# Kernel optimization log

Hardware: AMD Instinct MI355X
Metric: run time of the kernel (lower is better)

Reference implementation:

```python
import jax, jax.numpy as jnp
import numpy as np

T, B, I, H = 256, 128, 1024, 1024


def setup_inputs() -> dict:
    key = jax.random.key(0)
    ks = jax.random.split(key, 5)
    # weight init ranges per LSTMLayer.__init__ with wb=0 (no quantization):
    lim_hh = 1.0 / np.sqrt(H)
    lim_ih = 1.0 / np.sqrt(I)
    return {
        "x": jax.random.normal(ks[0], (T, B, I), dtype=jnp.float32),
        "h0": jax.random.normal(ks[1], (B, H), dtype=jnp.float32),
        "c0": jax.random.normal(ks[2], (B, H), dtype=jnp.float32),
        "W_ih": jax.random.uniform(ks[3], (4 * H, I), dtype=jnp.float32, minval=-lim_ih, maxval=lim_ih),
        "W_hh": jax.random.uniform(ks[4], (4 * H, H), dtype=jnp.float32, minval=-lim_hh, maxval=lim_hh),
        "b_ih": jnp.zeros((4 * H,), dtype=jnp.float32),   # uniform_(0, 0)
        "b_hh": jnp.ones((4 * H,), dtype=jnp.float32),    # uniform_(1, 1)
    }


def reference(x, h0, c0, W_ih, W_hh, b_ih, b_hh):
    # Standard LSTM cell, rolled over time with lax.scan.
    # gates layout follows torch LSTMCell: [i, f, g, o] chunks of size H.
    Wih_T = W_ih.T  # [I, 4H]
    Whh_T = W_hh.T  # [H, 4H]
    bias = b_ih + b_hh  # [4H]

    def step(carry, xt):
        h, c = carry  # [B,H] each
        gates = xt @ Wih_T + h @ Whh_T + bias  # [B, 4H]
        i, f, g, o = jnp.split(gates, 4, axis=-1)
        i = jax.nn.sigmoid(i)
        f = jax.nn.sigmoid(f)
        g = jnp.tanh(g)
        o = jax.nn.sigmoid(o)
        c_new = f * c + i * g
        h_new = o * jnp.tanh(c_new)
        return (h_new, c_new), h_new

    (hT, cT), ys = jax.lax.scan(step, (h0, c0), x)
    return ys, hT, cT  # ys: [T, B, H]
```

## Files before the change

### kernel.cpp

```cpp
#include <hip/hip_runtime.h>

#define T_ 256
#define B_ 128
#define I_ 1024
#define H_ 1024
#define G_ 4096
#define BH (B_*H_)
#define TB (T_*B_)

typedef float f32x4 __attribute__((ext_vector_type(4)));
typedef short bf16x8 __attribute__((ext_vector_type(8)));

__device__ inline unsigned short f2bf(float f) {
    union { float f; unsigned int u; } v; v.f = f;
    unsigned int u = v.u;
    unsigned int r = (u + 0x7fffu + ((u >> 16) & 1u)) >> 16;
    return (unsigned short)r;
}
__device__ inline float bf2f(unsigned short s) {
    union { unsigned int u; float f; } v; v.u = ((unsigned int)s) << 16;
    return v.f;
}
__device__ inline float sigmoidf_(float x) { return 1.0f / (1.0f + __expf(-x)); }
__device__ inline float tanhf_(float x) {
    x = fminf(15.0f, fmaxf(-15.0f, x));
    float e = __expf(2.0f * x);
    return (e - 1.0f) / (e + 1.0f);
}

__global__ void cvt_kernel(const float* __restrict__ src, unsigned short* __restrict__ dst, int n) {
    int i = (blockIdx.x * blockDim.x + threadIdx.x) * 4;
    int stride = gridDim.x * blockDim.x * 4;
    for (; i < n; i += stride) {
        float4 v = *reinterpret_cast<const float4*>(src + i);
        ushort4 o;
        o.x = f2bf(v.x); o.y = f2bf(v.y); o.z = f2bf(v.z); o.w = f2bf(v.w);
        *reinterpret_cast<ushort4*>(dst + i) = o;
    }
}

__global__ void bias_kernel(const float* __restrict__ a, const float* __restrict__ b, float* __restrict__ out) {
    int i = blockIdx.x * blockDim.x + threadIdx.x;
    if (i < G_) out[i] = a[i] + b[i];
}

__global__ __launch_bounds__(256) void pregemm(
    const unsigned short* __restrict__ xb,
    const unsigned short* __restrict__ wih,
    const float* __restrict__ bias,
    unsigned short* __restrict__ gx)
{
    int wgid = (blockIdx.x & 7) * 1024 + (blockIdx.x >> 3);
    int mg = wgid & 255;
    int ng = wgid >> 8;
    int m0 = mg * 128, n0 = ng * 128;
    int tid = threadIdx.x;
    int w = tid >> 6, l = tid & 63;
    int qm = (w >> 1) * 64, qn = (w & 1) * 64;
    int lr = l & 15, lk = (l >> 4) * 8, lq = l >> 4;

    const unsigned short* ap = xb  + (size_t)(m0 + qm + lr) * I_ + lk;
    const unsigned short* bp = wih + (size_t)(n0 + qn + lr) * I_ + lk;

    f32x4 acc[4][4] = {};
    #pragma unroll 4
    for (int kk = 0; kk < 32; ++kk) {
        bf16x8 a[4], b[4];
        #pragma unroll
        for (int mt = 0; mt < 4; ++mt)
            a[mt] = *reinterpret_cast<const bf16x8*>(ap + (size_t)mt * 16 * I_ + kk * 32);
        #pragma unroll
        for (int nt = 0; nt < 4; ++nt)
            b[nt] = *reinterpret_cast<const bf16x8*>(bp + (size_t)nt * 16 * I_ + kk * 32);
        #pragma unroll
        for (int mt = 0; mt < 4; ++mt)
            #pragma unroll
            for (int nt = 0; nt < 4; ++nt)
                acc[mt][nt] = __builtin_amdgcn_mfma_f32_16x16x32_bf16(a[mt], b[nt], acc[mt][nt], 0, 0, 0);
    }
    #pragma unroll
    for (int mt = 0; mt < 4; ++mt) {
        #pragma unroll
        for (int nt = 0; nt < 4; ++nt) {
            #pragma unroll
            for (int r = 0; r < 4; ++r) {
                int m = m0 + qm + mt * 16 + lq * 4 + r;
                int n = n0 + qn + nt * 16 + lr;
                gx[(size_t)m * G_ + n] = f2bf(acc[mt][nt][r] + bias[n]);
            }
        }
    }
}

__device__ __forceinline__ void group_barrier(unsigned* gbar, int step, int ing) {
    __syncthreads();
    if (threadIdx.x == 0) {
        unsigned target = (unsigned)(step * 8 + 7);
        unsigned old = __hip_atomic_fetch_add(gbar + (ing & 7) * 32, 1u,
                                              __ATOMIC_RELAXED, __HIP_MEMORY_SCOPE_AGENT);
        if (old == target) {
            unsigned mold = __hip_atomic_fetch_add(gbar + 256, 1u,
                                                   __ATOMIC_RELAXED, __HIP_MEMORY_SCOPE_AGENT);
            if (mold == target) {
                __hip_atomic_store(gbar + 288, (unsigned)(step + 1),
                                   __ATOMIC_RELAXED, __HIP_MEMORY_SCOPE_AGENT);
            }
        }
        while (__hip_atomic_load(gbar + 288, __ATOMIC_RELAXED, __HIP_MEMORY_SCOPE_AGENT)
               < (unsigned)(step + 1)) {
            __builtin_amdgcn_s_sleep(1);
        }
    }
    __syncthreads();
}

__global__ __launch_bounds__(512) void lstm_recur(
    const unsigned short* __restrict__ whh,
    const unsigned short* __restrict__ gx,
    const float* __restrict__ c0,
    unsigned short* __restrict__ hbuf,
    float* __restrict__ ys,
    float* __restrict__ hT, float* __restrict__ cT,
    unsigned* __restrict__ bar)
{
    __shared__ unsigned short whh_lds[8192 * 8];
    __shared__ float lds_g[4][32][16];

    const int bid = blockIdx.x;
    const int mg  = (bid & 7) >> 1;
    const int ing = (bid >> 3) * 2 + (bid & 1);
    const int m0 = mg * 32, n0 = ing * 16;
    unsigned* gbar = bar + mg * 512;

    const int tid = threadIdx.x;
    const int w = tid >> 6, l = tid & 63;
    const int mh = w >> 2, kq = w & 3;
    const int lr = l & 15, lkidx = l >> 4;

    for (int it = 0; it < 16; ++it) {
        int idx = it * 512 + tid;
        int row = idx >> 7;
        int ck  = idx & 127;
        int gg = row >> 4, cc = row & 15;
        bf16x8 v = *reinterpret_cast<const bf16x8*>(
            whh + (size_t)(gg * 1024 + n0 + cc) * H_ + ck * 8);
        *reinterpret_cast<bf16x8*>(whh_lds + ((size_t)ck * 64 + row) * 8) = v;
    }
    __syncthreads();

    const unsigned short* bwave = whh_lds + (((size_t)(kq * 32 + lkidx)) * 64 + lr) * 8;

    const int erow = tid >> 4, ecol = tid & 15;
    const size_t eoff = (size_t)(m0 + erow) * H_ + n0 + ecol;
    float c = c0[eoff];
    const unsigned short* gxp = gx + (size_t)(m0 + erow) * G_ + n0 + ecol;

    const size_t hrow = (size_t)(m0 + mh * 16 + lr) * H_ + kq * 256;

    unsigned short gx0 = gxp[0], gx1 = gxp[1024], gx2 = gxp[2048], gx3 = gxp[3072];

    for (int t = 0; t < T_; ++t) {
        const char* hpb = (const char*)hbuf
            + ((size_t)(t & 1) * BH + hrow) * 2 + lkidx * 16;
        bf16x8 hv0, hv1, hv2, hv3, hv4, hv5, hv6, hv7;
        asm volatile("global_load_dwordx4 %0, %1, off sc0 sc1"             : "=&v"(hv0) : "v"(hpb));
        asm volatile("global_load_dwordx4 %0, %1, off offset:64 sc0 sc1"   : "=&v"(hv1) : "v"(hpb));
        asm volatile("global_load_dwordx4 %0, %1, off offset:128 sc0 sc1"  : "=&v"(hv2) : "v"(hpb));
        asm volatile("global_load_dwordx4 %0, %1, off offset:192 sc0 sc1"  : "=&v"(hv3) : "v"(hpb));
        asm volatile("global_load_dwordx4 %0, %1, off offset:256 sc0 sc1"  : "=&v"(hv4) : "v"(hpb));
        asm volatile("global_load_dwordx4 %0, %1, off offset:320 sc0 sc1"  : "=&v"(hv5) : "v"(hpb));
        asm volatile("global_load_dwordx4 %0, %1, off offset:384 sc0 sc1"  : "=&v"(hv6) : "v"(hpb));
        asm volatile("global_load_dwordx4 %0, %1, off offset:448 sc0 sc1"  : "=&v"(hv7) : "v"(hpb));

        {
            float* lg = (float*)lds_g;
            lg[tid] = 0.f; lg[tid + 512] = 0.f; lg[tid + 1024] = 0.f; lg[tid + 1536] = 0.f;
        }

        asm volatile("s_waitcnt vmcnt(0)" ::: "memory");
        __builtin_amdgcn_sched_barrier(0);

        f32x4 acc[4] = {};
#define MFMA_K(KK, HV)                                                              \
        {                                                                           \
            _Pragma("unroll")                                                       \
            for (int g4 = 0; g4 < 4; ++g4) {                                        \
                bf16x8 bb = *reinterpret_cast<const bf16x8*>(                       \
                    bwave + (KK) * 2048 + g4 * 128);                                \
                acc[g4] = __builtin_amdgcn_mfma_f32_16x16x32_bf16(                  \
                    HV, bb, acc[g4], 0, 0, 0);                                      \
            }                                                                       \
        }
        MFMA_K(0, hv0) MFMA_K(1, hv1) MFMA_K(2, hv2) MFMA_K(3, hv3)
        MFMA_K(4, hv4) MFMA_K(5, hv5) MFMA_K(6, hv6) MFMA_K(7, hv7)
#undef MFMA_K
        __syncthreads();

        #pragma unroll
        for (int g4 = 0; g4 < 4; ++g4)
            #pragma unroll
            for (int r = 0; r < 4; ++r)
                atomicAdd(&lds_g[g4][mh * 16 + lkidx * 4 + r][lr], acc[g4][r]);
        __syncthreads();

        float gi = lds_g[0][erow][ecol] + bf2f(gx0);
        float gf = lds_g[1][erow][ecol] + bf2f(gx1);
        float gg = lds_g[2][erow][ecol] + bf2f(gx2);
        float go = lds_g[3][erow][ecol] + bf2f(gx3);
        float iv = sigmoidf_(gi);
        float fv = sigmoidf_(gf);
        float gv = tanhf_(gg);
        float ov = sigmoidf_(go);
        c = fv * c + iv * gv;
        float hn = ov * tanhf_(c);

        ys[(size_t)t * BH + eoff] = hn;

        unsigned short* hbn = hbuf + (size_t)((t + 1) & 1) * BH;
        float hn_o = __shfl_xor(hn, 1);
        if ((tid & 1) == 0) {
            unsigned u = (unsigned)f2bf(hn) | (((unsigned)f2bf(hn_o)) << 16);
            __hip_atomic_store((unsigned*)(hbn + eoff), u,
                               __ATOMIC_RELAXED, __HIP_MEMORY_SCOPE_AGENT);
        }
        if (t == T_ - 1) { hT[eoff] = hn; cT[eoff] = c; }

        if (t + 1 < T_) {
            const unsigned short* p = gxp + (size_t)(t + 1) * B_ * G_;
            gx0 = p[0]; gx1 = p[1024]; gx2 = p[2048]; gx3 = p[3072];
            group_barrier(gbar, t, ing);
        }
    }
}

extern "C" void kernel_launch(void* const* d_in, const int* in_sizes, int n_in,
                              void* d_out, int out_size, void* d_ws, size_t ws_size,
                              hipStream_t stream)
{
    const float* x   = (const float*)d_in[0];
    const float* h0  = (const float*)d_in[1];
    const float* c0  = (const float*)d_in[2];
    const float* Wih = (const float*)d_in[3];
    const float* Whh = (const float*)d_in[4];
    const float* bih = (const float*)d_in[5];
    const float* bhh = (const float*)d_in[6];

    char* ws = (char*)d_ws;
    unsigned short* gx   = (unsigned short*)(ws);
    unsigned short* xb   = (unsigned short*)(ws + 268435456);
    unsigned short* wihb = (unsigned short*)(ws + 335544320);
    unsigned short* whhb = (unsigned short*)(ws + 343932928);
    unsigned short* hbuf = (unsigned short*)(ws + 352321536);
    float*          bias = (float*)(ws + 352845824);
    unsigned*       bar  = (unsigned*)(ws + 352862208);

    float* out = (float*)d_out;
    float* ys = out;
    float* hT = out + (size_t)TB * H_;
    float* cT = hT + BH;

    hipMemsetAsync(bar, 0, 8192, stream);
    cvt_kernel<<<2048, 256, 0, stream>>>(x,   xb,   TB * I_);
    cvt_kernel<<<512,  256, 0, stream>>>(Wih, wihb, G_ * I_);
    cvt_kernel<<<512,  256, 0, stream>>>(Whh, whhb, G_ * H_);
    cvt_kernel<<<128,  256, 0, stream>>>(h0,  hbuf, BH);
    bias_kernel<<<16, 256, 0, stream>>>(bih, bhh, bias);

    pregemm<<<8192, 256, 0, stream>>>(xb, wihb, bias, gx);

    lstm_recur<<<256, 512, 0, stream>>>(whhb, gx, c0, hbuf, ys, hT, cT, bar);
}
```

Measured before the change: 4.834 ms.

## Stage pregemm tiles through LDS and replace tree barrier with per-wave counter polling

The input-projection GEMM now double-buffers A/B tiles into LDS using direct global-to-LDS loads, with two blocks per CU, instead of each wave streaming fragments straight from global memory. The recurrent kernel drops the hierarchical atomic group barrier. Each block increments one of 8 leaf counters per step, and each wave polls only the two counters covering the K-quarter of h it will read. This removes the serial master-counter hop and the block-wide wait before loading h. The trade-off is more polling traffic and dependence on relaxed-ordering visibility of the h stores. The ys store is also moved after the h publish.

```diff
diff --git a/kernel.cpp b/kernel.cpp
--- a/kernel.cpp
+++ b/kernel.cpp
@@ -26,6 +26,13 @@
     x = fminf(15.0f, fmaxf(-15.0f, x));
     float e = __expf(2.0f * x);
     return (e - 1.0f) / (e + 1.0f);
+}
+
+__device__ __forceinline__ void gload16(const unsigned short* g, unsigned short* l) {
+    __builtin_amdgcn_global_load_lds(
+        (const __attribute__((address_space(1))) void*)g,
+        (__attribute__((address_space(3))) void*)l,
+        16, 0, 0);
 }
 
 __global__ void cvt_kernel(const float* __restrict__ src, unsigned short* __restrict__ dst, int n) {
@@ -44,40 +51,70 @@
     if (i < G_) out[i] = a[i] + b[i];
 }
 
-__global__ __launch_bounds__(256) void pregemm(
+__global__ __launch_bounds__(256, 2) void pregemm(
     const unsigned short* __restrict__ xb,
     const unsigned short* __restrict__ wih,
     const float* __restrict__ bias,
     unsigned short* __restrict__ gx)
 {
-    int wgid = (blockIdx.x & 7) * 1024 + (blockIdx.x >> 3);
-    int mg = wgid & 255;
-    int ng = wgid >> 8;
+    __shared__ unsigned short Ab[2][128 * 64];
+    __shared__ unsigned short Bb[2][128 * 64];
+
+    int swz = (blockIdx.x & 7) * 1024 + (blockIdx.x >> 3);
+    int mg = swz & 255;
+    int ng = swz >> 8;
     int m0 = mg * 128, n0 = ng * 128;
     int tid = threadIdx.x;
     int w = tid >> 6, l = tid & 63;
     int qm = (w >> 1) * 64, qn = (w & 1) * 64;
-    int lr = l & 15, lk = (l >> 4) * 8, lq = l >> 4;
-
-    const unsigned short* ap = xb  + (size_t)(m0 + qm + lr) * I_ + lk;
-    const unsigned short* bp = wih + (size_t)(n0 + qn + lr) * I_ + lk;
+    int lr = l & 15, lkidx = (l >> 4);
+
+    int srow = ((w * 4) * 64 + l) >> 3;
+    int sk8  = l & 7;
+
+#define STAGE(BUF, KT)                                                              \
+    {                                                                               \
+        _Pragma("unroll")                                                           \
+        for (int it = 0; it < 4; ++it) {                                            \
+            int row = srow + it * 8;                                                \
+            gload16(xb  + (size_t)(m0 + row) * I_ + (KT) * 64 + sk8 * 8,            \
+                    &Ab[BUF][(w * 4 + it) * 512]);                                  \
+            gload16(wih + (size_t)(n0 + row) * I_ + (KT) * 64 + sk8 * 8,            \
+                    &Bb[BUF][(w * 4 + it) * 512]);                                  \
+        }                                                                           \
+    }
 
     f32x4 acc[4][4] = {};
-    #pragma unroll 4
-    for (int kk = 0; kk < 32; ++kk) {
-        bf16x8 a[4], b[4];
+    int buf = 0;
+    STAGE(0, 0)
+    __syncthreads();
+
+    for (int kt = 0; kt < 16; ++kt) {
+        if (kt + 1 < 16) STAGE(buf ^ 1, kt + 1)
         #pragma unroll
-        for (int mt = 0; mt < 4; ++mt)
-            a[mt] = *reinterpret_cast<const bf16x8*>(ap + (size_t)mt * 16 * I_ + kk * 32);
-        #pragma unroll
-        for (int nt = 0; nt < 4; ++nt)
-            b[nt] = *reinterpret_cast<const bf16x8*>(bp + (size_t)nt * 16 * I_ + kk * 32);
-        #pragma unroll
-        for (int mt = 0; mt < 4; ++mt)
+        for (int kk = 0; kk < 2; ++kk) {
+            bf16x8 a[4], b[4];
+            #pragma unroll
+            for (int mt = 0; mt < 4; ++mt)
+                a[mt] = *reinterpret_cast<const bf16x8*>(
+                    &Ab[buf][(qm + mt * 16 + lr) * 64 + kk * 32 + lkidx * 8]);
             #pragma unroll
             for (int nt = 0; nt < 4; ++nt)
-                acc[mt][nt] = __builtin_amdgcn_mfma_f32_16x16x32_bf16(a[mt], b[nt], acc[mt][nt], 0, 0, 0);
-    }
+                b[nt] = *reinterpret_cast<const bf16x8*>(
+                    &Bb[buf][(qn + nt * 16 + lr) * 64 + kk * 32 + lkidx * 8]);
+            #pragma unroll
+            for (int mt = 0; mt < 4; ++mt)
+                #pragma unroll
+                for (int nt = 0; nt < 4; ++nt)
+                    acc[mt][nt] = __builtin_amdgcn_mfma_f32_16x16x32_bf16(
+                        a[mt], b[nt], acc[mt][nt], 0, 0, 0);
+        }
+        __syncthreads();
+        buf ^= 1;
+    }
+#undef STAGE
+
+    int lq = l >> 4;
     #pragma unroll
     for (int mt = 0; mt < 4; ++mt) {
         #pragma unroll
@@ -90,28 +127,6 @@
             }
         }
     }
-}
-
-__device__ __forceinline__ void group_barrier(unsigned* gbar, int step, int ing) {
-    __syncthreads();
-    if (threadIdx.x == 0) {
-        unsigned target = (unsigned)(step * 8 + 7);
-        unsigned old = __hip_atomic_fetch_add(gbar + (ing & 7) * 32, 1u,
-                                              __ATOMIC_RELAXED, __HIP_MEMORY_SCOPE_AGENT);
-        if (old == target) {
-            unsigned mold = __hip_atomic_fetch_add(gbar + 256, 1u,
-                                                   __ATOMIC_RELAXED, __HIP_MEMORY_SCOPE_AGENT);
-            if (mold == target) {
-                __hip_atomic_store(gbar + 288, (unsigned)(step + 1),
-                                   __ATOMIC_RELAXED, __HIP_MEMORY_SCOPE_AGENT);
-            }
-        }
-        while (__hip_atomic_load(gbar + 288, __ATOMIC_RELAXED, __HIP_MEMORY_SCOPE_AGENT)
-               < (unsigned)(step + 1)) {
-            __builtin_amdgcn_s_sleep(1);
-        }
-    }
-    __syncthreads();
 }
 
 __global__ __launch_bounds__(512) void lstm_recur(
@@ -130,12 +145,14 @@
     const int mg  = (bid & 7) >> 1;
     const int ing = (bid >> 3) * 2 + (bid & 1);
     const int m0 = mg * 32, n0 = ing * 16;
-    unsigned* gbar = bar + mg * 512;
 
     const int tid = threadIdx.x;
     const int w = tid >> 6, l = tid & 63;
     const int mh = w >> 2, kq = w & 3;
     const int lr = l & 15, lkidx = l >> 4;
+
+    const unsigned* pollw = bar + mg * 32 + 2 * kq;
+    unsigned* leafw = bar + mg * 32 + (ing >> 3);
 
     for (int it = 0; it < 16; ++it) {
         int idx = it * 512 + tid;
@@ -160,6 +177,18 @@
     unsigned short gx0 = gxp[0], gx1 = gxp[1024], gx2 = gxp[2048], gx3 = gxp[3072];
 
     for (int t = 0; t < T_; ++t) {
+        if (t > 0) {
+            unsigned tgt = 8u * (unsigned)t;
+            while (true) {
+                unsigned long long lv;
+                asm volatile("global_load_dwordx2 %0, %1, off sc0 sc1"
+                             : "=&v"(lv) : "v"(pollw));
+                asm volatile("s_waitcnt vmcnt(0)" ::: "memory");
+                if ((unsigned)lv >= tgt && (unsigned)(lv >> 32) >= tgt) break;
+                __builtin_amdgcn_s_sleep(1);
+            }
+        }
+
         const char* hpb = (const char*)hbuf
             + ((size_t)(t & 1) * BH + hrow) * 2 + lkidx * 16;
         bf16x8 hv0, hv1, hv2, hv3, hv4, hv5, hv6, hv7;
@@ -214,8 +243,6 @@
         c = fv * c + iv * gv;
         float hn = ov * tanhf_(c);
 
-        ys[(size_t)t * BH + eoff] = hn;
-
         unsigned short* hbn = hbuf + (size_t)((t + 1) & 1) * BH;
         float hn_o = __shfl_xor(hn, 1);
         if ((tid & 1) == 0) {
@@ -223,12 +250,20 @@
             __hip_atomic_store((unsigned*)(hbn + eoff), u,
                                __ATOMIC_RELAXED, __HIP_MEMORY_SCOPE_AGENT);
         }
+        ys[(size_t)t * BH + eoff] = hn;
         if (t == T_ - 1) { hT[eoff] = hn; cT[eoff] = c; }
 
         if (t + 1 < T_) {
             const unsigned short* p = gxp + (size_t)(t + 1) * B_ * G_;
             gx0 = p[0]; gx1 = p[1024]; gx2 = p[2048]; gx3 = p[3072];
-            group_barrier(gbar, t, ing);
+        }
+
+        __syncthreads();
+
+        if (tid == 0 && t + 1 < T_) {
+            unsigned one = 1u;
+            asm volatile("global_atomic_add %0, %1, off"
+                         :: "v"(leafw), "v"(one) : "memory");
         }
     }
 }
@@ -259,7 +294,7 @@
     float* hT = out + (size_t)TB * H_;
     float* cT = hT + BH;
 
-    hipMemsetAsync(bar, 0, 8192, stream);
+    hipMemsetAsync(bar, 0, 4096, stream);
     cvt_kernel<<<2048, 256, 0, stream>>>(x,   xb,   TB * I_);
     cvt_kernel<<<512,  256, 0, stream>>>(Wih, wihb, G_ * I_);
     cvt_kernel<<<512,  256, 0, stream>>>(Whh, whhb, G_ * H_);
```

Result: faster. 4.345 ms (-10.1%).
